# Optimization experiments

Hardware: AMD Instinct MI355X
Metric: run time of the kernel (lower is better)

## Reference

```python
import jax, jax.numpy as jnp
import numpy as np

DIM = 256          # channel dim
WIN = 16           # window_size
PW = WIN // 2      # permuted_window_size
N = PW * PW        # tokens per window = 64
H = 8              # num_heads
KV_DIM = DIM // 2  # compressed q/k/v dim = 128
HD = KV_DIM // H   # per-head compressed dim = 16
SCALE = (DIM // H) ** (-0.5)  # NOTE: scale uses UNcompressed head dim, as in source
B = 4096           # total windows (batch * num_windows)
NW = 64            # nw_mask; B % NW == 0


def _relative_position_index():
    coords = np.stack(np.meshgrid(np.arange(PW), np.arange(PW), indexing='ij'))  # [2,PW,PW]
    cf = coords.reshape(2, -1)                          # [2, N]
    rel = cf[:, :, None] - cf[:, None, :]               # [2, N, N]
    rel = rel.transpose(1, 2, 0).copy()                 # [N, N, 2]
    rel[:, :, 0] += PW - 1
    rel[:, :, 1] += PW - 1
    rel[:, :, 0] *= 2 * PW - 1
    return jnp.asarray(rel.sum(-1), dtype=jnp.int32)    # [N, N]


def setup_inputs() -> dict:
    key = jax.random.key(0)
    ks = jax.random.split(key, 9)
    std = 0.02
    return {
        'x': jax.random.normal(ks[0], (B, N, DIM), dtype=jnp.float32),
        'mask': jax.random.normal(ks[1], (NW, N, N), dtype=jnp.float32),
        'q_w': jax.random.normal(ks[2], (KV_DIM, DIM), dtype=jnp.float32) * std,
        'q_b': jnp.zeros((KV_DIM,), dtype=jnp.float32),
        'kv_w': jax.random.normal(ks[3], (2 * KV_DIM, DIM), dtype=jnp.float32) * std,
        'kv_b': jnp.zeros((2 * KV_DIM,), dtype=jnp.float32),
        'proj_w': jax.random.normal(ks[4], (DIM, KV_DIM), dtype=jnp.float32) * std,
        'proj_b': jnp.zeros((DIM,), dtype=jnp.float32),
        'bias_table': jax.random.normal(ks[5], ((2 * PW - 1) ** 2, H), dtype=jnp.float32) * std,
        'rel_index': _relative_position_index(),
    }


def reference(x, mask, q_w, q_b, kv_w, kv_b, proj_w, proj_b, bias_table, rel_index):
    b, n, c = x.shape
    # compressed Q and KV projections
    q = (x @ q_w.T + q_b).reshape(b, n, H, HD).transpose(0, 2, 1, 3)        # [B,H,N,HD]
    kv = (x @ kv_w.T + kv_b).reshape(b, n, 2, H, HD).transpose(2, 0, 3, 1, 4)
    k, v = kv[0], kv[1]                                                     # [B,H,N,HD]
    attn = jnp.einsum('bhnd,bhmd->bhnm', q, k) * SCALE                      # [B,H,N,N]
    # relative position bias gather
    bias = bias_table[rel_index.reshape(-1)].reshape(n, n, H).transpose(2, 0, 1)  # [H,N,N]
    attn = attn + bias[None]
    # window mask add: broadcast mask over (B//NW) window-batches and heads
    attn = attn.reshape(b // NW, NW, H, n, n) + mask[None, :, None]
    attn = attn.reshape(b, H, n, n)
    attn = jax.nn.softmax(attn, axis=-1)
    out = jnp.einsum('bhnm,bhmd->bhnd', attn, v)                            # [B,H,N,HD]
    out = out.transpose(0, 2, 1, 3).reshape(b, n, KV_DIM)
    return out @ proj_w.T + proj_b                                          # [B,N,DIM]
```

## Files before the change

kernel.cpp:

```cpp
#include <hip/hip_runtime.h>


typedef unsigned short u16;
typedef short bf16x8 __attribute__((ext_vector_type(8)));
typedef short bf16x4 __attribute__((ext_vector_type(4)));
typedef float f32x4  __attribute__((ext_vector_type(4)));

__device__ __forceinline__ f32x4 mfma_bf16(bf16x8 a, bf16x8 b, f32x4 c) {
  return __builtin_amdgcn_mfma_f32_16x16x32_bf16(a, b, c, 0, 0, 0);
}

#define SCALE_F 0.1767766952966369f

__device__ __forceinline__ u16 f2b(float f) {
  unsigned u = __builtin_bit_cast(unsigned, f);
  u = (u + 0x7FFFu + ((u >> 16) & 1u)) >> 16;
  return (u16)u;
}
__device__ __forceinline__ float b2f(u16 h) {
  return __builtin_bit_cast(float, (unsigned)h << 16);
}

#define WS_WQKV   0
#define WS_WPROJ  98304
#define WS_BIASPK 131072
#define WS_MASKPK 163840
#define WS_QKVB   425984
#define WS_TOTAL  426368

__global__ void psa_prep(const float* __restrict__ qw, const float* __restrict__ qb,
                         const float* __restrict__ kvw, const float* __restrict__ kvb,
                         const float* __restrict__ projw, const float* __restrict__ bt,
                         const int* __restrict__ ri, const float* __restrict__ mask,
                         u16* __restrict__ ws) {
  int i = blockIdx.x * 256 + threadIdx.x;
  if (i < 98304) {
    int r = i >> 8, c = i & 255;
    ws[WS_WQKV + i] = f2b(r < 128 ? qw[r * 256 + c] : kvw[(r - 128) * 256 + c]);
  } else if (i < 131072) {
    int j = i - 98304;
    ws[WS_WPROJ + j] = f2b(projw[j]);
  } else if (i < 163840) {
    int j = i - 131072;
    int t = j & 15, lane = (j >> 4) & 63, w = (j >> 10) & 3, h = j >> 12;
    int row = w * 16 + (lane >> 4) * 4 + (t & 3);
    int col = (t >> 2) * 16 + (lane & 15);
    ws[WS_BIASPK + j] = f2b(bt[ri[row * 64 + col] * 8 + h]);
  } else if (i < 425984) {
    int j = i - 163840;
    int t = j & 15, lane = (j >> 4) & 63, w = (j >> 10) & 3, nw = j >> 12;
    int row = w * 16 + (lane >> 4) * 4 + (t & 3);
    int col = (t >> 2) * 16 + (lane & 15);
    ws[WS_MASKPK + j] = f2b(mask[(nw * 64 + row) * 64 + col]);
  } else if (i < WS_TOTAL) {
    int j = i - 425984;
    ws[WS_QKVB + j] = f2b(j < 128 ? qb[j] : kvb[j - 128]);
  }
}

__global__ __launch_bounds__(256, 2) void psa_main(
    const float* __restrict__ x, const float* __restrict__ proj_b,
    const u16* __restrict__ ws, float* __restrict__ out) {
  __shared__ u16 qks[64 * 264];
  __shared__ u16 vsm[8 * 16 * 72];
  __shared__ u16 scr[64 * 72];

  const int win = blockIdx.x;
  const int tid = threadIdx.x;
  const int wave = tid >> 6;
  const int lane = tid & 63;
  const int quad = lane >> 4;
  const int n16  = lane & 15;
  const int nw   = win & 63;

  const f32x4 zero4 = {0.f, 0.f, 0.f, 0.f};
  const float* xw = x + (size_t)win * 16384;

  f32x4 acc[6][4];
  #pragma unroll
  for (int nt = 0; nt < 6; ++nt)
    #pragma unroll
    for (int mt = 0; mt < 4; ++mt) acc[nt][mt] = zero4;

  const int col0 = wave * 96;
  for (int kc = 0; kc < 4; ++kc) {
    __syncthreads();
    #pragma unroll
    for (int it = 0; it < 4; ++it) {
      int idx = it * 256 + tid;
      int row = idx >> 4, c4 = (idx & 15) * 4;
      float4 v = *(const float4*)(xw + row * 256 + kc * 64 + c4);
      bf16x4 pk;
      pk[0] = (short)f2b(v.x); pk[1] = (short)f2b(v.y);
      pk[2] = (short)f2b(v.z); pk[3] = (short)f2b(v.w);
      *(bf16x4*)&scr[row * 72 + c4] = pk;
    }
    __syncthreads();
    #pragma unroll
    for (int ks = 0; ks < 2; ++ks) {
      bf16x8 af[4];
      #pragma unroll
      for (int mt = 0; mt < 4; ++mt)
        af[mt] = *(const bf16x8*)&scr[(mt * 16 + n16) * 72 + ks * 32 + quad * 8];
      #pragma unroll
      for (int nt = 0; nt < 6; ++nt) {
        bf16x8 bw = *(const bf16x8*)&ws[WS_WQKV + (col0 + nt * 16 + n16) * 256 + kc * 64 + ks * 32 + quad * 8];
        #pragma unroll
        for (int mt = 0; mt < 4; ++mt) acc[nt][mt] = mfma_bf16(af[mt], bw, acc[nt][mt]);
      }
    }
  }
  #pragma unroll
  for (int nt = 0; nt < 6; ++nt) {
    int col = col0 + nt * 16 + n16;
    float badd = b2f(ws[WS_QKVB + col]);
    if (col < 256) {
      #pragma unroll
      for (int mt = 0; mt < 4; ++mt)
        #pragma unroll
        for (int r = 0; r < 4; ++r)
          qks[(mt * 16 + quad * 4 + r) * 264 + col] = f2b(acc[nt][mt][r] + badd);
    } else {
      int vc = col - 256, vh = vc >> 4, vd = vc & 15;
      #pragma unroll
      for (int mt = 0; mt < 4; ++mt)
        #pragma unroll
        for (int r = 0; r < 4; ++r)
          vsm[vh * 1152 + vd * 72 + mt * 16 + quad * 4 + r] = f2b(acc[nt][mt][r] + badd);
    }
  }
  __syncthreads();

  const int kq = (quad & 1) * 8;
  const u16* bpk = ws + WS_BIASPK + (wave * 64 + lane) * 16;
  const u16* mpk = ws + WS_MASKPK + ((nw * 4 + wave) * 64 + lane) * 16;
  bf16x8 mm0 = *(const bf16x8*)mpk;
  bf16x8 mm1 = *(const bf16x8*)(mpk + 8);

  #pragma unroll 1
  for (int h = 0; h < 8; ++h) {
    bf16x8 aq = (bf16x8){0, 0, 0, 0, 0, 0, 0, 0};
    if (quad < 2) aq = *(const bf16x8*)&qks[(wave * 16 + n16) * 264 + h * 16 + kq];
    f32x4 s[4];
    #pragma unroll
    for (int nt = 0; nt < 4; ++nt) {
      bf16x8 bk = (bf16x8){0, 0, 0, 0, 0, 0, 0, 0};
      if (quad < 2) bk = *(const bf16x8*)&qks[(nt * 16 + n16) * 264 + 128 + h * 16 + kq];
      s[nt] = mfma_bf16(aq, bk, zero4);
    }
    bf16x8 bm0 = *(const bf16x8*)(bpk + h * 4096);
    bf16x8 bm1 = *(const bf16x8*)(bpk + h * 4096 + 8);

    float pe[4][4];
    float rinv[4];
    #pragma unroll
    for (int r = 0; r < 4; ++r) {
      float l[4];
      #pragma unroll
      for (int nt = 0; nt < 4; ++nt) {
        int t = nt * 4 + r;
        float bv = b2f((u16)(t < 8 ? bm0[t] : bm1[t - 8]));
        float mv = b2f((u16)(t < 8 ? mm0[t] : mm1[t - 8]));
        l[nt] = s[nt][r] * SCALE_F + bv + mv;
      }
      float mx = fmaxf(fmaxf(l[0], l[1]), fmaxf(l[2], l[3]));
      mx = fmaxf(mx, __shfl_xor(mx, 1));
      mx = fmaxf(mx, __shfl_xor(mx, 2));
      mx = fmaxf(mx, __shfl_xor(mx, 4));
      mx = fmaxf(mx, __shfl_xor(mx, 8));
      float sum = 0.f;
      #pragma unroll
      for (int nt = 0; nt < 4; ++nt) {
        float e = __expf(l[nt] - mx);
        pe[nt][r] = e; sum += e;
      }
      sum += __shfl_xor(sum, 1);
      sum += __shfl_xor(sum, 2);
      sum += __shfl_xor(sum, 4);
      sum += __shfl_xor(sum, 8);
      rinv[r] = __builtin_amdgcn_rcpf(sum);
      #pragma unroll
      for (int nt = 0; nt < 4; ++nt)
        scr[(wave * 16 + quad * 4 + r) * 72 + nt * 16 + n16] = f2b(pe[nt][r]);
    }
    f32x4 o = zero4;
    #pragma unroll
    for (int ks = 0; ks < 2; ++ks) {
      bf16x8 ap = *(const bf16x8*)&scr[(wave * 16 + n16) * 72 + ks * 32 + quad * 8];
      bf16x8 bv = *(const bf16x8*)&vsm[h * 1152 + n16 * 72 + ks * 32 + quad * 8];
      o = mfma_bf16(ap, bv, o);
    }
    #pragma unroll
    for (int r = 0; r < 4; ++r)
      qks[(wave * 16 + quad * 4 + r) * 264 + h * 16 + n16] = f2b(o[r] * rinv[r]);
  }
  __syncthreads();

  f32x4 po[4][4];
  #pragma unroll
  for (int nt = 0; nt < 4; ++nt)
    #pragma unroll
    for (int mt = 0; mt < 4; ++mt) po[nt][mt] = zero4;
  #pragma unroll
  for (int ks = 0; ks < 4; ++ks) {
    bf16x8 af[4];
    #pragma unroll
    for (int mt = 0; mt < 4; ++mt)
      af[mt] = *(const bf16x8*)&qks[(mt * 16 + n16) * 264 + ks * 32 + quad * 8];
    #pragma unroll
    for (int nt = 0; nt < 4; ++nt) {
      bf16x8 bw = *(const bf16x8*)&ws[WS_WPROJ + (wave * 64 + nt * 16 + n16) * 128 + ks * 32 + quad * 8];
      #pragma unroll
      for (int mt = 0; mt < 4; ++mt) po[nt][mt] = mfma_bf16(af[mt], bw, po[nt][mt]);
    }
  }
  float* ow = out + (size_t)win * 16384;
  #pragma unroll
  for (int nt = 0; nt < 4; ++nt) {
    int coln = wave * 64 + nt * 16 + n16;
    float pb = proj_b[coln];
    #pragma unroll
    for (int mt = 0; mt < 4; ++mt)
      #pragma unroll
      for (int r = 0; r < 4; ++r)
        ow[(mt * 16 + quad * 4 + r) * 256 + coln] = po[nt][mt][r] + pb;
  }
}

extern "C" void kernel_launch(void* const* d_in, const int* in_sizes, int n_in,
                              void* d_out, int out_size, void* d_ws, size_t ws_size,
                              hipStream_t stream) {
  (void)in_sizes; (void)n_in; (void)out_size; (void)ws_size;
  const float* x    = (const float*)d_in[0];
  const float* mask = (const float*)d_in[1];
  const float* qw   = (const float*)d_in[2];
  const float* qb   = (const float*)d_in[3];
  const float* kvw  = (const float*)d_in[4];
  const float* kvb  = (const float*)d_in[5];
  const float* pw   = (const float*)d_in[6];
  const float* pb   = (const float*)d_in[7];
  const float* bt   = (const float*)d_in[8];
  const int*   ri   = (const int*)d_in[9];
  u16* ws = (u16*)d_ws;

  psa_prep<<<(WS_TOTAL + 255) / 256, 256, 0, stream>>>(qw, qb, kvw, kvb, pw, bt, ri, mask, ws);
  psa_main<<<4096, 256, 0, stream>>>(x, pb, ws, (float*)d_out);
}
```

Baseline: 642.7 us.

## Compute transposed scores in registers, drop max-subtraction, stage full x tile once

New measurement: 566.2 us. -11.9%, faster.

```diff
diff --git a/kernel.cpp b/kernel.cpp
--- a/kernel.cpp
+++ b/kernel.cpp
@@ -9,8 +9,19 @@
 __device__ __forceinline__ f32x4 mfma_bf16(bf16x8 a, bf16x8 b, f32x4 c) {
   return __builtin_amdgcn_mfma_f32_16x16x32_bf16(a, b, c, 0, 0, 0);
 }
+__device__ __forceinline__ f32x4 mfma16(bf16x4 a, bf16x4 b, f32x4 c) {
+#if __has_builtin(__builtin_amdgcn_mfma_f32_16x16x16bf16_1k)
+  return __builtin_amdgcn_mfma_f32_16x16x16bf16_1k(a, b, c, 0, 0, 0);
+#else
+  f32x4 d;
+  asm("v_mfma_f32_16x16x16_bf16 %0, %1, %2, %3" : "=v"(d) : "v"(a), "v"(b), "v"(c));
+  return d;
+#endif
+}
 
 #define SCALE_F 0.1767766952966369f
+#define LOG2E_F 1.4426950408889634f
+#define C2F (SCALE_F * LOG2E_F)
 
 __device__ __forceinline__ u16 f2b(float f) {
   unsigned u = __builtin_bit_cast(unsigned, f);
@@ -19,6 +30,13 @@
 }
 __device__ __forceinline__ float b2f(u16 h) {
   return __builtin_bit_cast(float, (unsigned)h << 16);
+}
+__device__ __forceinline__ float fexp2(float x) {
+#if __has_builtin(__builtin_amdgcn_exp2f)
+  return __builtin_amdgcn_exp2f(x);
+#else
+  return __expf(x * 0.6931471805599453f);
+#endif
 }
 
 #define WS_WQKV   0
@@ -43,27 +61,26 @@
   } else if (i < 163840) {
     int j = i - 131072;
     int t = j & 15, lane = (j >> 4) & 63, w = (j >> 10) & 3, h = j >> 12;
-    int row = w * 16 + (lane >> 4) * 4 + (t & 3);
-    int col = (t >> 2) * 16 + (lane & 15);
-    ws[WS_BIASPK + j] = f2b(bt[ri[row * 64 + col] * 8 + h]);
+    int row = w * 16 + (lane & 15);
+    int col = (t >> 2) * 16 + ((lane >> 4) & 3) * 4 + (t & 3);
+    ws[WS_BIASPK + j] = f2b(LOG2E_F * bt[ri[row * 64 + col] * 8 + h]);
   } else if (i < 425984) {
     int j = i - 163840;
     int t = j & 15, lane = (j >> 4) & 63, w = (j >> 10) & 3, nw = j >> 12;
-    int row = w * 16 + (lane >> 4) * 4 + (t & 3);
-    int col = (t >> 2) * 16 + (lane & 15);
-    ws[WS_MASKPK + j] = f2b(mask[(nw * 64 + row) * 64 + col]);
+    int row = w * 16 + (lane & 15);
+    int col = (t >> 2) * 16 + ((lane >> 4) & 3) * 4 + (t & 3);
+    ws[WS_MASKPK + j] = f2b(LOG2E_F * mask[(nw * 64 + row) * 64 + col]);
   } else if (i < WS_TOTAL) {
     int j = i - 425984;
     ws[WS_QKVB + j] = f2b(j < 128 ? qb[j] : kvb[j - 128]);
   }
 }
 
-__global__ __launch_bounds__(256, 2) void psa_main(
+__global__ __launch_bounds__(256, 3) void psa_main(
     const float* __restrict__ x, const float* __restrict__ proj_b,
     const u16* __restrict__ ws, float* __restrict__ out) {
-  __shared__ u16 qks[64 * 264];
-  __shared__ u16 vsm[8 * 16 * 72];
-  __shared__ u16 scr[64 * 72];
+  __shared__ __align__(16) u16 qks[64 * 264];
+  __shared__ __align__(16) u16 vsm[8 * 16 * 72];
 
   const int win = blockIdx.x;
   const int tid = threadIdx.x;
@@ -76,6 +93,18 @@
   const f32x4 zero4 = {0.f, 0.f, 0.f, 0.f};
   const float* xw = x + (size_t)win * 16384;
 
+  #pragma unroll
+  for (int it = 0; it < 16; ++it) {
+    int idx = it * 256 + tid;
+    int row = idx >> 6, c4 = (idx & 63) * 4;
+    float4 v = *(const float4*)(xw + row * 256 + c4);
+    bf16x4 pk;
+    pk[0] = (short)f2b(v.x); pk[1] = (short)f2b(v.y);
+    pk[2] = (short)f2b(v.z); pk[3] = (short)f2b(v.w);
+    *(bf16x4*)&qks[row * 264 + c4] = pk;
+  }
+  __syncthreads();
+
   f32x4 acc[6][4];
   #pragma unroll
   for (int nt = 0; nt < 6; ++nt)
@@ -83,33 +112,21 @@
     for (int mt = 0; mt < 4; ++mt) acc[nt][mt] = zero4;
 
   const int col0 = wave * 96;
-  for (int kc = 0; kc < 4; ++kc) {
-    __syncthreads();
-    #pragma unroll
-    for (int it = 0; it < 4; ++it) {
-      int idx = it * 256 + tid;
-      int row = idx >> 4, c4 = (idx & 15) * 4;
-      float4 v = *(const float4*)(xw + row * 256 + kc * 64 + c4);
-      bf16x4 pk;
-      pk[0] = (short)f2b(v.x); pk[1] = (short)f2b(v.y);
-      pk[2] = (short)f2b(v.z); pk[3] = (short)f2b(v.w);
-      *(bf16x4*)&scr[row * 72 + c4] = pk;
-    }
-    __syncthreads();
-    #pragma unroll
-    for (int ks = 0; ks < 2; ++ks) {
-      bf16x8 af[4];
-      #pragma unroll
-      for (int mt = 0; mt < 4; ++mt)
-        af[mt] = *(const bf16x8*)&scr[(mt * 16 + n16) * 72 + ks * 32 + quad * 8];
-      #pragma unroll
-      for (int nt = 0; nt < 6; ++nt) {
-        bf16x8 bw = *(const bf16x8*)&ws[WS_WQKV + (col0 + nt * 16 + n16) * 256 + kc * 64 + ks * 32 + quad * 8];
-        #pragma unroll
-        for (int mt = 0; mt < 4; ++mt) acc[nt][mt] = mfma_bf16(af[mt], bw, acc[nt][mt]);
-      }
-    }
-  }
+  #pragma unroll 2
+  for (int kk = 0; kk < 8; ++kk) {
+    bf16x8 af[4];
+    #pragma unroll
+    for (int mt = 0; mt < 4; ++mt)
+      af[mt] = *(const bf16x8*)&qks[(mt * 16 + n16) * 264 + kk * 32 + quad * 8];
+    #pragma unroll
+    for (int nt = 0; nt < 6; ++nt) {
+      bf16x8 bw = *(const bf16x8*)&ws[WS_WQKV + (col0 + nt * 16 + n16) * 256 + kk * 32 + quad * 8];
+      #pragma unroll
+      for (int mt = 0; mt < 4; ++mt) acc[nt][mt] = mfma_bf16(af[mt], bw, acc[nt][mt]);
+    }
+  }
+  __syncthreads();
+
   #pragma unroll
   for (int nt = 0; nt < 6; ++nt) {
     int col = col0 + nt * 16 + n16;
@@ -131,7 +148,6 @@
   }
   __syncthreads();
 
-  const int kq = (quad & 1) * 8;
   const u16* bpk = ws + WS_BIASPK + (wave * 64 + lane) * 16;
   const u16* mpk = ws + WS_MASKPK + ((nw * 4 + wave) * 64 + lane) * 16;
   bf16x8 mm0 = *(const bf16x8*)mpk;
@@ -139,60 +155,51 @@
 
   #pragma unroll 1
   for (int h = 0; h < 8; ++h) {
-    bf16x8 aq = (bf16x8){0, 0, 0, 0, 0, 0, 0, 0};
-    if (quad < 2) aq = *(const bf16x8*)&qks[(wave * 16 + n16) * 264 + h * 16 + kq];
+    bf16x4 qf = *(const bf16x4*)&qks[(wave * 16 + n16) * 264 + h * 16 + quad * 4];
     f32x4 s[4];
     #pragma unroll
     for (int nt = 0; nt < 4; ++nt) {
-      bf16x8 bk = (bf16x8){0, 0, 0, 0, 0, 0, 0, 0};
-      if (quad < 2) bk = *(const bf16x8*)&qks[(nt * 16 + n16) * 264 + 128 + h * 16 + kq];
-      s[nt] = mfma_bf16(aq, bk, zero4);
+      bf16x4 kf = *(const bf16x4*)&qks[(nt * 16 + n16) * 264 + 128 + h * 16 + quad * 4];
+      s[nt] = mfma16(kf, qf, zero4);
     }
     bf16x8 bm0 = *(const bf16x8*)(bpk + h * 4096);
     bf16x8 bm1 = *(const bf16x8*)(bpk + h * 4096 + 8);
 
-    float pe[4][4];
-    float rinv[4];
-    #pragma unroll
-    for (int r = 0; r < 4; ++r) {
-      float l[4];
-      #pragma unroll
-      for (int nt = 0; nt < 4; ++nt) {
-        int t = nt * 4 + r;
-        float bv = b2f((u16)(t < 8 ? bm0[t] : bm1[t - 8]));
-        float mv = b2f((u16)(t < 8 ? mm0[t] : mm1[t - 8]));
-        l[nt] = s[nt][r] * SCALE_F + bv + mv;
+    float e[4][4];
+    float sum = 0.f;
+    #pragma unroll
+    for (int nt = 0; nt < 4; ++nt)
+      #pragma unroll
+      for (int r = 0; r < 4; ++r) {
+        int j = nt * 4 + r;
+        float bv = b2f((u16)(j < 8 ? bm0[j] : bm1[j - 8]));
+        float mv = b2f((u16)(j < 8 ? mm0[j] : mm1[j - 8]));
+        float ev = fexp2(s[nt][r] * C2F + (bv + mv));
+        e[nt][r] = ev;
+        sum += ev;
       }
-      float mx = fmaxf(fmaxf(l[0], l[1]), fmaxf(l[2], l[3]));
-      mx = fmaxf(mx, __shfl_xor(mx, 1));
-      mx = fmaxf(mx, __shfl_xor(mx, 2));
-      mx = fmaxf(mx, __shfl_xor(mx, 4));
-      mx = fmaxf(mx, __shfl_xor(mx, 8));
-      float sum = 0.f;
-      #pragma unroll
-      for (int nt = 0; nt < 4; ++nt) {
-        float e = __expf(l[nt] - mx);
-        pe[nt][r] = e; sum += e;
-      }
-      sum += __shfl_xor(sum, 1);
-      sum += __shfl_xor(sum, 2);
-      sum += __shfl_xor(sum, 4);
-      sum += __shfl_xor(sum, 8);
-      rinv[r] = __builtin_amdgcn_rcpf(sum);
-      #pragma unroll
-      for (int nt = 0; nt < 4; ++nt)
-        scr[(wave * 16 + quad * 4 + r) * 72 + nt * 16 + n16] = f2b(pe[nt][r]);
+    sum += __shfl_xor(sum, 16);
+    sum += __shfl_xor(sum, 32);
+    float rinv = __builtin_amdgcn_rcpf(sum);
+
+    bf16x4 pf[4];
+    #pragma unroll
+    for (int nt = 0; nt < 4; ++nt) {
+      bf16x4 t;
+      #pragma unroll
+      for (int r = 0; r < 4; ++r) t[r] = (short)f2b(e[nt][r]);
+      pf[nt] = t;
     }
     f32x4 o = zero4;
     #pragma unroll
-    for (int ks = 0; ks < 2; ++ks) {
-      bf16x8 ap = *(const bf16x8*)&scr[(wave * 16 + n16) * 72 + ks * 32 + quad * 8];
-      bf16x8 bv = *(const bf16x8*)&vsm[h * 1152 + n16 * 72 + ks * 32 + quad * 8];
-      o = mfma_bf16(ap, bv, o);
-    }
-    #pragma unroll
-    for (int r = 0; r < 4; ++r)
-      qks[(wave * 16 + quad * 4 + r) * 264 + h * 16 + n16] = f2b(o[r] * rinv[r]);
+    for (int kt = 0; kt < 4; ++kt) {
+      bf16x4 vf = *(const bf16x4*)&vsm[h * 1152 + n16 * 72 + kt * 16 + quad * 4];
+      o = mfma16(vf, pf[kt], o);
+    }
+    bf16x4 ov;
+    #pragma unroll
+    for (int r = 0; r < 4; ++r) ov[r] = (short)f2b(o[r] * rinv);
+    *(bf16x4*)&qks[(wave * 16 + n16) * 264 + h * 16 + quad * 4] = ov;
   }
   __syncthreads();
 
```
